# Optimization experiments

Measured on AMD Instinct MI355X. Metric: run time of the kernel, lower is better.

The kernel has to match this reference:

```python
import jax, jax.numpy as jnp
import numpy as np

DIM = 1024
HEADS = 16
DIM_HEAD = 64
INNER = HEADS * DIM_HEAD  # 1024
B, N = 2, 2048


def setup_inputs() -> dict:
    key = jax.random.key(0)
    ks = jax.random.split(key, 6)
    x = jax.random.normal(ks[0], (B, N, DIM), dtype=jnp.float32)
    rel_pos_bias = jax.random.normal(ks[1], (1, HEADS, N, N), dtype=jnp.float32)
    g = jnp.ones((DIM,), dtype=jnp.float32)
    # Linear weights stored torch-style as [out_features, in_features].
    # Note: original zero-inits Wo; we use small random values so outputs/grads are non-trivial.
    Wq = jax.random.normal(ks[2], (INNER, DIM), dtype=jnp.float32) * (DIM ** -0.5)
    Wkv = jax.random.normal(ks[3], (2 * INNER, DIM), dtype=jnp.float32) * (DIM ** -0.5)
    Wo = jax.random.normal(ks[4], (DIM, INNER), dtype=jnp.float32) * (INNER ** -0.5)
    return {"x": x, "rel_pos_bias": rel_pos_bias, "g": g, "Wq": Wq, "Wkv": Wkv, "Wo": Wo}


def reference(x, rel_pos_bias, g, Wq, Wkv, Wo):
    eps = 1e-5  # x is float32
    # Faithful to source: normalize over dim=1 (sequence axis), biased variance.
    mean = jnp.mean(x, axis=1, keepdims=True)          # [b, 1, d]
    var = jnp.var(x, axis=1, keepdims=True)            # [b, 1, d]
    xn = (x - mean) * jax.lax.rsqrt(jnp.maximum(var, eps)) * g

    q = xn @ Wq.T                                      # [b, n, inner]
    kv = xn @ Wkv.T                                    # [b, n, 2*inner]
    k, v = jnp.split(kv, 2, axis=-1)

    def to_heads(t):  # b n (h d) -> b h n d
        b, n, _ = t.shape
        return t.reshape(b, n, HEADS, DIM_HEAD).transpose(0, 2, 1, 3)

    q, k, v = to_heads(q), to_heads(k), to_heads(v)
    q = q * (DIM_HEAD ** -0.5)

    sim = jnp.einsum('bhid,bhjd->bhij', q, k) + rel_pos_bias  # [b, h, n, n]
    attn = jax.nn.softmax(sim, axis=-1)
    out = jnp.einsum('bhij,bhjd->bhid', attn, v)              # [b, h, n, d]
    out = out.transpose(0, 2, 1, 3).reshape(x.shape[0], x.shape[1], INNER)
    return out @ Wo.T                                         # [b, n, dim]
```

## Files before the change

kernel.cpp:

```cpp
#include <hip/hip_runtime.h>
#include <hip/hip_bf16.h>

typedef __bf16 bf16;
typedef __attribute__((ext_vector_type(8))) __bf16 bf16x8;
typedef __attribute__((ext_vector_type(4))) __bf16 bf16x4;
typedef __attribute__((ext_vector_type(4))) float f32x4;
typedef __attribute__((ext_vector_type(16))) float f32x16;
typedef __attribute__((ext_vector_type(4))) unsigned int u32x4;

#define DIMD  1024
#define SEQ   2048
#define BATCH 2
#define HEADS 16
#define INNER 1024
#define QKVN  3072
#define ROWS  (BATCH*SEQ)
#define LOG2E 1.44269504f

__global__ void ln_partial(const float* __restrict__ x,
                           float* __restrict__ psum, float* __restrict__ psq) {
    const int nc = blockIdx.x;
    const int b  = blockIdx.y;
    const int t  = threadIdx.x;
    const float* xp = x + ((size_t)b*SEQ + (size_t)nc*32)*DIMD;
    float s0=0,s1=0,s2=0,s3=0,q0=0,q1=0,q2=0,q3=0;
    for (int r=0; r<32; ++r) {
        const float* row = xp + (size_t)r*DIMD;
        float v0=row[t], v1=row[t+256], v2=row[t+512], v3=row[t+768];
        s0+=v0; q0+=v0*v0; s1+=v1; q1+=v1*v1;
        s2+=v2; q2+=v2*v2; s3+=v3; q3+=v3*v3;
    }
    float* ps = psum + ((size_t)b*64 + nc)*DIMD;
    float* pq = psq  + ((size_t)b*64 + nc)*DIMD;
    ps[t]=s0; ps[t+256]=s1; ps[t+512]=s2; ps[t+768]=s3;
    pq[t]=q0; pq[t+256]=q1; pq[t+512]=q2; pq[t+768]=q3;
}

__global__ void ln_finalize(const float* __restrict__ psum, const float* __restrict__ psq,
                            const float* __restrict__ g,
                            float* __restrict__ scale, float* __restrict__ shift) {
    const int d = blockIdx.x*256 + threadIdx.x;
    const int b = blockIdx.y;
    float s=0.f, q=0.f;
    for (int nc=0; nc<64; ++nc) {
        s += psum[((size_t)b*64+nc)*DIMD + d];
        q += psq [((size_t)b*64+nc)*DIMD + d];
    }
    const float inv_n = 1.f/(float)SEQ;
    float mean = s*inv_n;
    float var  = q*inv_n - mean*mean;
    var = fmaxf(var, 1e-5f);
    scale[b*DIMD+d] = g[d]*rsqrtf(var);
    shift[b*DIMD+d] = mean;
}

__global__ void ln_apply(const float* __restrict__ x,
                         const float* __restrict__ scale, const float* __restrict__ shift,
                         bf16* __restrict__ xn) {
    size_t idx = ((size_t)blockIdx.x*256 + threadIdx.x)*4;
    int b = (int)(idx >> 21);
    int d = (int)(idx & (DIMD-1));
    f32x4 v  = *reinterpret_cast<const f32x4*>(x + idx);
    f32x4 sc = *reinterpret_cast<const f32x4*>(scale + (size_t)b*DIMD + d);
    f32x4 sh = *reinterpret_cast<const f32x4*>(shift + (size_t)b*DIMD + d);
    bf16x4 o;
    o.x = (bf16)((v.x - sh.x)*sc.x);
    o.y = (bf16)((v.y - sh.y)*sc.y);
    o.z = (bf16)((v.z - sh.z)*sc.z);
    o.w = (bf16)((v.w - sh.w)*sc.w);
    *reinterpret_cast<bf16x4*>(xn + idx) = o;
}

__global__ void castk(const float* __restrict__ s, bf16* __restrict__ d, int n, float scl) {
    int i = (blockIdx.x*256 + threadIdx.x)*4;
    if (i >= n) return;
    f32x4 v = *reinterpret_cast<const f32x4*>(s + i);
    bf16x4 o; o.x=(bf16)(v.x*scl); o.y=(bf16)(v.y*scl); o.z=(bf16)(v.z*scl); o.w=(bf16)(v.w*scl);
    *reinterpret_cast<bf16x4*>(d + i) = o;
}

__device__ __forceinline__ void gload16(const void* g, void* l) {
    __builtin_amdgcn_global_load_lds(
        (const __attribute__((address_space(1))) unsigned int*)g,
        (__attribute__((address_space(3))) unsigned int*)l,
        16, 0, 0);
}

__device__ inline void store_out(float* p, float v) { *p = v; }
__device__ inline void store_out(bf16*  p, float v) { *p = (bf16)v; }

template <typename OT>
__global__ __launch_bounds__(256, 2)
void gemm_bt(const bf16* __restrict__ A, const bf16* __restrict__ B,
             OT* __restrict__ C, int M, int N, int K) {
    __shared__ bf16 As[128*64];
    __shared__ bf16 Bs[128*64];
    const int t = threadIdx.x;
    const int wave = t >> 6, lane = t & 63;
    const int wr = wave >> 1, wc = wave & 1;
    const int m0 = blockIdx.y*128, n0 = blockIdx.x*128;
    const int lr = lane & 15, lg = lane >> 4;
    const int srow = wave*32 + (lane>>3);
    const int scol = (lane&7)*8;

    f32x4 acc[4][4];
    #pragma unroll
    for (int i=0;i<4;++i)
        #pragma unroll
        for (int j=0;j<4;++j) acc[i][j] = (f32x4){0.f,0.f,0.f,0.f};

    for (int k0=0; k0<K; k0+=64) {
        #pragma unroll
        for (int i=0;i<4;++i) {
            gload16(A + (size_t)(m0+srow+8*i)*K + k0 + scol, As + (srow+8*i)*64 + scol);
            gload16(B + (size_t)(n0+srow+8*i)*K + k0 + scol, Bs + (srow+8*i)*64 + scol);
        }
        __syncthreads();
        #pragma unroll
        for (int kk=0; kk<2; ++kk) {
            bf16x8 a[4], b[4];
            #pragma unroll
            for (int mi=0;mi<4;++mi)
                a[mi] = *reinterpret_cast<const bf16x8*>(As + (wr*64+mi*16+lr)*64 + kk*32+lg*8);
            #pragma unroll
            for (int ni=0;ni<4;++ni)
                b[ni] = *reinterpret_cast<const bf16x8*>(Bs + (wc*64+ni*16+lr)*64 + kk*32+lg*8);
            #pragma unroll
            for (int mi=0;mi<4;++mi)
                #pragma unroll
                for (int ni=0;ni<4;++ni)
                    acc[mi][ni] = __builtin_amdgcn_mfma_f32_16x16x32_bf16(a[mi], b[ni], acc[mi][ni], 0, 0, 0);
        }
        __syncthreads();
    }
    #pragma unroll
    for (int mi=0;mi<4;++mi)
        #pragma unroll
        for (int ni=0;ni<4;++ni)
            #pragma unroll
            for (int r=0;r<4;++r) {
                int row = m0 + wr*64 + mi*16 + lg*4 + r;
                int col = n0 + wc*64 + ni*16 + lr;
                store_out(&C[(size_t)row*N + col], acc[mi][ni][r]);
            }
}

__global__ __launch_bounds__(256)
void transpose_v(const bf16* __restrict__ qkv, bf16* __restrict__ vT) {
    __shared__ bf16 tile[64][72];
    const int nt = blockIdx.x, h = blockIdx.y, b = blockIdx.z;
    const int t = threadIdx.x;
    const bf16* src = qkv + ((size_t)(b*SEQ + nt*64))*QKVN + 2*INNER + h*64;
    #pragma unroll
    for (int i=0;i<2;++i) {
        int c = t + 256*i, row = c>>3, col = (c&7)*8;
        *reinterpret_cast<bf16x8*>(&tile[row][col]) =
            *reinterpret_cast<const bf16x8*>(src + (size_t)row*QKVN + col);
    }
    __syncthreads();
    bf16* dst = vT + ((size_t)(b*HEADS + h))*64*SEQ + nt*64;
    #pragma unroll
    for (int i=0;i<2;++i) {
        int c = t + 256*i, d = c>>3, n0 = (c&7)*8;
        bf16x8 v;
        #pragma unroll
        for (int j=0;j<8;++j) v[j] = tile[n0+j][d];
        *reinterpret_cast<bf16x8*>(dst + (size_t)d*SEQ + n0) = v;
    }
}


__device__ __forceinline__ unsigned pk2(float a, float b) {
    union { bf16 h[2]; unsigned u; } x;
    x.h[0] = (bf16)a; x.h[1] = (bf16)b;
    return x.u;
}

#define ATTN_BARRIER()                                         \
    __builtin_amdgcn_sched_barrier(0);                         \
    asm volatile("s_waitcnt lgkmcnt(0)" ::: "memory");         \
    __builtin_amdgcn_s_barrier();                              \
    __builtin_amdgcn_sched_barrier(0)

#define ATTN_ITER(CUR, T)                                                          \
  {                                                                                \
              \
    if ((T)+1 < 32) {                                                              \
      *reinterpret_cast<bf16x8*>(&Ks[0][(CUR)^1][st_off])  = krA;                  \
      *reinterpret_cast<bf16x8*>(&Ks[1][(CUR)^1][st_off])  = krB;                  \
      *reinterpret_cast<bf16x8*>(&VTs[0][(CUR)^1][st_off]) = vrA;                  \
      *reinterpret_cast<bf16x8*>(&VTs[1][(CUR)^1][st_off]) = vrB;                  \
      _Pragma("unroll")                                                            \
      for (int i=0;i<4;++i)                                                        \
        *reinterpret_cast<f32x4*>(&BsL[(CUR)^1][bst[i]]) = breg[i];                \
    }                                                                              \
                      \
    if ((T)+2 < 32) {                                                              \
      krA = *reinterpret_cast<const bf16x8*>(kbase0 + (size_t)(((T)+2)*64+srow)*QKVN + scol);  \
      krB = *reinterpret_cast<const bf16x8*>(kbase1 + (size_t)(((T)+2)*64+srow)*QKVN + scol);  \
      vrA = *reinterpret_cast<const bf16x8*>(vtb0 + (size_t)srow*SEQ + ((T)+2)*64 + scol);     \
      vrB = *reinterpret_cast<const bf16x8*>(vtb1 + (size_t)srow*SEQ + ((T)+2)*64 + scol);     \
      _Pragma("unroll")                                                            \
      for (int i=0;i<4;++i)                                                        \
        breg[i] = *reinterpret_cast<const f32x4*>(bgl + (size_t)(32*i)*SEQ + ((T)+2)*64);      \
    }                                                                              \
                                    \
    f32x16 p0 = (f32x16)(0.0f), p1 = (f32x16)(0.0f);                               \
    __builtin_amdgcn_s_setprio(1);                                                 \
    _Pragma("unroll")                                                              \
    for (int s=0;s<4;++s) {                                                        \
      bf16x8 kf0 = *reinterpret_cast<const bf16x8*>(&myK[(CUR)*4096 + koff[0][s]]); \
      p0 = __builtin_amdgcn_mfma_f32_32x32x16_bf16(kf0, qf[s], p0, 0,0,0);         \
      bf16x8 kf1 = *reinterpret_cast<const bf16x8*>(&myK[(CUR)*4096 + koff[1][s]]); \
      p1 = __builtin_amdgcn_mfma_f32_32x32x16_bf16(kf1, qf[s], p1, 0,0,0);         \
    }                                                                              \
    __builtin_amdgcn_s_setprio(0);                                                 \
                              \
    f32x4 bb0[4], bb1[4];                                                          \
    _Pragma("unroll")                                                              \
    for (int rr=0;rr<4;++rr) {                                                     \
      bb0[rr] = *reinterpret_cast<const f32x4*>(&BsL[CUR][brd[0][rr]]);            \
      bb1[rr] = *reinterpret_cast<const f32x4*>(&BsL[CUR][brd[1][rr]]);            \
    }                                                                              \
            \
    float v0[16], v1[16];                                                          \
    _Pragma("unroll")                                                              \
    for (int r=0;r<16;++r) {                                                       \
      v0[r] = __builtin_fmaf(bb0[r>>2][r&3], LOG2E, p0[r]);                        \
      v1[r] = __builtin_fmaf(bb1[r>>2][r&3], LOG2E, p1[r]);                        \
    }                                                                              \
    float mx[8];                                                                   \
    _Pragma("unroll")                                                              \
    for (int i=0;i<8;++i)                                                          \
      mx[i] = fmaxf(fmaxf(v0[i], v0[i+8]), fmaxf(v1[i], v1[i+8]));                 \
    _Pragma("unroll")                                                              \
    for (int i=0;i<4;++i) mx[i] = fmaxf(mx[i], mx[i+4]);                           \
    float vmax = fmaxf(fmaxf(mx[0],mx[2]), fmaxf(mx[1],mx[3]));                    \
    vmax = fmaxf(vmax, __shfl_xor(vmax, 32));                                      \
    if (!__all(vmax <= m + 11.5f)) {                                               \
      float mnew = fmaxf(m, vmax);                                                 \
      float sc = __builtin_amdgcn_exp2f(m - mnew);                                 \
      m = mnew; l *= sc;                                                           \
      _Pragma("unroll")                                                            \
      for (int r=0;r<16;++r) {                                                     \
        float scr = __shfl(sc, (r&3)+8*(r>>2)+4*hi);                               \
        accO0[r] *= scr; accO1[r] *= scr;                                          \
      }                                                                            \
    }                                                                              \
    float e0[16], e1[16];                                                          \
    _Pragma("unroll")                                                              \
    for (int r=0;r<16;++r) {                                                       \
      e0[r] = __builtin_amdgcn_exp2f(v0[r] - m);                                   \
      e1[r] = __builtin_amdgcn_exp2f(v1[r] - m);                                   \
    }                                                                              \
    float sm[8];                                                                   \
    _Pragma("unroll")                                                              \
    for (int i=0;i<8;++i) sm[i] = (e0[i]+e0[i+8]) + (e1[i]+e1[i+8]);               \
    _Pragma("unroll")                                                              \
    for (int i=0;i<4;++i) sm[i] += sm[i+4];                                        \
    float rsum = (sm[0]+sm[2]) + (sm[1]+sm[3]);                                    \
    rsum += __shfl_xor(rsum, 32);                                                  \
    l += rsum;                                                                     \
           \
    unsigned W0[4][2], W1[4][2];                                                   \
    _Pragma("unroll")                                                              \
    for (int rr=0;rr<4;++rr) {                                                     \
      W0[rr][0] = pk2(e0[4*rr+0], e0[4*rr+1]);                                     \
      W0[rr][1] = pk2(e0[4*rr+2], e0[4*rr+3]);                                     \
      W1[rr][0] = pk2(e1[4*rr+0], e1[4*rr+1]);                                     \
      W1[rr][1] = pk2(e1[4*rr+2], e1[4*rr+3]);                                     \
    }                                                                              \
                               \
    bf16x8 pa[4];                                                                  \
    _Pragma("unroll")                                                              \
    for (int s4=0;s4<4;++s4) {                                                     \
      unsigned u[4];                                                               \
      _Pragma("unroll")                                                            \
      for (int hh=0;hh<2;++hh) {                                                   \
        unsigned a0 = (s4>>1) ? W1[2*(s4&1)  ][hh] : W0[2*(s4&1)  ][hh];           \
        unsigned a1 = (s4>>1) ? W1[2*(s4&1)+1][hh] : W0[2*(s4&1)+1][hh];           \
        unsigned X = hi ? a0 : a1;                                                 \
        unsigned R = (unsigned)__shfl_xor((int)X, 32);                             \
        u[hh]   = hi ? R  : a0;                                                    \
        u[2+hh] = hi ? a1 : R;                                                     \
      }                                                                            \
      u32x4 uv = {u[0], u[1], u[2], u[3]};                                         \
      pa[s4] = __builtin_bit_cast(bf16x8, uv);                                     \
    }                                                                              \
                                                                        \
    __builtin_amdgcn_s_setprio(1);                                                 \
    _Pragma("unroll")                                                              \
    for (int s4=0;s4<4;++s4) {                                                     \
      bf16x8 vfa = *reinterpret_cast<const bf16x8*>(&myV[(CUR)*4096 + voff[0][s4]]); \
      accO0 = __builtin_amdgcn_mfma_f32_32x32x16_bf16(pa[s4], vfa, accO0, 0,0,0);  \
      bf16x8 vfb = *reinterpret_cast<const bf16x8*>(&myV[(CUR)*4096 + voff[1][s4]]); \
      accO1 = __builtin_amdgcn_mfma_f32_32x32x16_bf16(pa[s4], vfb, accO1, 0,0,0);  \
    }                                                                              \
    __builtin_amdgcn_s_setprio(0);                                                 \
    ATTN_BARRIER();                                                                \
  }

__global__ __launch_bounds__(512, 1)
void attn_kernel(const bf16* __restrict__ qkv, const bf16* __restrict__ vTg,
                 const float* __restrict__ bias, bf16* __restrict__ oh) {
    __shared__ bf16 Ks[2][2][64*64];
    __shared__ bf16 VTs[2][2][64*64];
    __shared__ float BsL[2][128*64];

    const int qt = blockIdx.x, h = blockIdx.y;
    const int t = threadIdx.x;
    const int w = t >> 6, lane = t & 63;
    const int wb = w >> 2;
    const int wq = w & 3;
    const int ql = lane & 31, hi = lane >> 5;
    const int q0 = qt*128;

    int koff[2][4], voff[2][4];
    #pragma unroll
    for (int B2=0;B2<2;++B2)
        #pragma unroll
        for (int s=0;s<4;++s) {
            koff[B2][s] = (32*B2+ql)*64 + (((2*s+hi) ^ (ql&7))*8);
            voff[B2][s] = (32*B2+ql)*64 + (((2*s+hi) ^ (ql&7))*8);
        }
    bf16* myK = (bf16*)Ks[wb];
    bf16* myV = (bf16*)VTs[wb];

    int bst[4];
    {
        int rlow = t>>4;
        int swg  = ((t&15) ^ (rlow&15))*4;
        #pragma unroll
        for (int i=0;i<4;++i)
            bst[i] = (32*i + rlow)*64 + swg;
    }
    int brd[2][4];
    #pragma unroll
    for (int B2=0;B2<2;++B2)
        #pragma unroll
        for (int rr=0;rr<4;++rr)
            brd[B2][rr] = (wq*32+ql)*64 + (((8*B2+2*rr+hi) ^ (ql&15))*4);

    const int srow = t>>3;
    const int scol = (t&7)*8;
    const int st_off = srow*64 + (((t&7) ^ (srow&7))*8);

    const bf16* qrow = qkv + ((size_t)(wb*SEQ + q0 + wq*32 + ql))*QKVN + h*64 + hi*8;
    bf16x8 qf[4];
    #pragma unroll
    for (int s=0;s<4;++s)
        qf[s] = *reinterpret_cast<const bf16x8*>(qrow + 16*s);

    const bf16* kbase0 = qkv + INNER + h*64;
    const bf16* kbase1 = qkv + (size_t)SEQ*QKVN + INNER + h*64;
    const bf16* vtb0   = vTg + (size_t)h*64*SEQ;
    const bf16* vtb1   = vTg + (size_t)(HEADS + h)*64*SEQ;
    const float* bgl = bias + ((size_t)h*SEQ + (size_t)(q0 + (t>>4)))*SEQ + 4*(t&15);

    bf16x8 krA, krB, vrA, vrB;
    f32x4 breg[4];

    *reinterpret_cast<bf16x8*>(&Ks[0][0][st_off]) =
        *reinterpret_cast<const bf16x8*>(kbase0 + (size_t)srow*QKVN + scol);
    *reinterpret_cast<bf16x8*>(&Ks[1][0][st_off]) =
        *reinterpret_cast<const bf16x8*>(kbase1 + (size_t)srow*QKVN + scol);
    *reinterpret_cast<bf16x8*>(&VTs[0][0][st_off]) =
        *reinterpret_cast<const bf16x8*>(vtb0 + (size_t)srow*SEQ + scol);
    *reinterpret_cast<bf16x8*>(&VTs[1][0][st_off]) =
        *reinterpret_cast<const bf16x8*>(vtb1 + (size_t)srow*SEQ + scol);
    #pragma unroll
    for (int i=0;i<4;++i)
        breg[i] = *reinterpret_cast<const f32x4*>(bgl + (size_t)(32*i)*SEQ);
    #pragma unroll
    for (int i=0;i<4;++i)
        *reinterpret_cast<f32x4*>(&BsL[0][bst[i]]) = breg[i];
    krA = *reinterpret_cast<const bf16x8*>(kbase0 + (size_t)(64+srow)*QKVN + scol);
    krB = *reinterpret_cast<const bf16x8*>(kbase1 + (size_t)(64+srow)*QKVN + scol);
    vrA = *reinterpret_cast<const bf16x8*>(vtb0 + (size_t)srow*SEQ + 64 + scol);
    vrB = *reinterpret_cast<const bf16x8*>(vtb1 + (size_t)srow*SEQ + 64 + scol);
    #pragma unroll
    for (int i=0;i<4;++i)
        breg[i] = *reinterpret_cast<const f32x4*>(bgl + (size_t)(32*i)*SEQ + 64);
    ATTN_BARRIER();

    float m = -__builtin_inff();
    float l = 0.f;
    f32x16 accO0 = (f32x16)(0.0f), accO1 = (f32x16)(0.0f);

    for (int t2 = 0; t2 < 32; t2 += 2) {
        ATTN_ITER(0, t2);
        ATTN_ITER(1, t2+1);
    }

    float linv = 1.f/l;
    bf16* ob = oh + ((size_t)(wb*SEQ + q0 + wq*32))*INNER + h*64 + ql;
    #pragma unroll
    for (int r=0;r<16;++r) {
        int qoff = (r&3) + 8*(r>>2) + 4*hi;
        float li = __shfl(linv, qoff);
        ob[(size_t)qoff*INNER]      = (bf16)(accO0[r]*li);
        ob[(size_t)qoff*INNER + 32] = (bf16)(accO1[r]*li);
    }
}

extern "C" void kernel_launch(void* const* d_in, const int* in_sizes, int n_in,
                              void* d_out, int out_size, void* d_ws, size_t ws_size,
                              hipStream_t stream) {
    const float* x    = (const float*)d_in[0];
    const float* bias = (const float*)d_in[1];
    const float* g    = (const float*)d_in[2];
    const float* Wq   = (const float*)d_in[3];
    const float* Wkv  = (const float*)d_in[4];
    const float* Wo   = (const float*)d_in[5];
    float* out = (float*)d_out;

    char* ws = (char*)d_ws;
    bf16*  xn    = (bf16*)(ws);
    bf16*  vT    = (bf16*)(ws);
    bf16*  wqkv  = (bf16*)(ws + 8388608);
    bf16*  wo    = (bf16*)(ws + 14680064);
    bf16*  qkv   = (bf16*)(ws + 16777216);
    bf16*  oh    = (bf16*)(ws + 41943040);
    float* psum  = (float*)(ws + 50331648);
    float* psq   = (float*)(ws + 50855936);
    float* scale = (float*)(ws + 51380224);
    float* shift = (float*)(ws + 51388416);

    ln_partial <<<dim3(64,2), 256, 0, stream>>>(x, psum, psq);
    ln_finalize<<<dim3(4,2),  256, 0, stream>>>(psum, psq, g, scale, shift);
    ln_apply   <<<dim3(4096), 256, 0, stream>>>(x, scale, shift, xn);

    castk<<<dim3(1024), 256, 0, stream>>>(Wq,  wqkv,           1048576, 0.125f*LOG2E);
    castk<<<dim3(2048), 256, 0, stream>>>(Wkv, wqkv + 1048576, 2097152, 1.0f);
    castk<<<dim3(1024), 256, 0, stream>>>(Wo,  wo,             1048576, 1.0f);

    gemm_bt<bf16><<<dim3(24,32), 256, 0, stream>>>(xn, wqkv, qkv, ROWS, QKVN, DIMD);

    transpose_v<<<dim3(32,16,2), 256, 0, stream>>>(qkv, vT);

    attn_kernel<<<dim3(16,16), 512, 0, stream>>>(qkv, vT, bias, oh);

    gemm_bt<float><<<dim3(8,32), 256, 0, stream>>>(oh, wo, out, ROWS, INNER, INNER);
}
```

Baseline: 181.6 us.

## Stage attention K/V/bias tiles with direct global-to-LDS loads and fuse weight casts

The attention kernel no longer copies K, V^T and bias tiles through registers into LDS. It issues global_load_lds DMA into the swizzled double buffers one tile ahead, and each iteration's barrier now waits on vmcnt as well. This frees registers and removes LDS store instructions, but the prefetch distance shrinks from two tiles to one, so every iteration must drain its global loads. Separately, the three weight-cast launches are merged into one kernel to save launch overhead.

```diff
diff --git a/kernel.cpp b/kernel.cpp
--- a/kernel.cpp
+++ b/kernel.cpp
@@ -71,12 +71,19 @@
     *reinterpret_cast<bf16x4*>(xn + idx) = o;
 }
 
-__global__ void castk(const float* __restrict__ s, bf16* __restrict__ d, int n, float scl) {
+__global__ void castk_all(const float* __restrict__ Wq, const float* __restrict__ Wkv,
+                          const float* __restrict__ Wo,
+                          bf16* __restrict__ wqkv, bf16* __restrict__ wo, float qs) {
     int i = (blockIdx.x*256 + threadIdx.x)*4;
-    if (i >= n) return;
-    f32x4 v = *reinterpret_cast<const f32x4*>(s + i);
-    bf16x4 o; o.x=(bf16)(v.x*scl); o.y=(bf16)(v.y*scl); o.z=(bf16)(v.z*scl); o.w=(bf16)(v.w*scl);
-    *reinterpret_cast<bf16x4*>(d + i) = o;
+    f32x4 v; bf16* dst;
+    if (i < 1048576)      { v = *reinterpret_cast<const f32x4*>(Wq + i);
+                            v.x*=qs; v.y*=qs; v.z*=qs; v.w*=qs; dst = wqkv + i; }
+    else if (i < 3145728) { v = *reinterpret_cast<const f32x4*>(Wkv + (i-1048576));
+                            dst = wqkv + i; }
+    else                  { v = *reinterpret_cast<const f32x4*>(Wo + (i-3145728));
+                            dst = wo + (i-3145728); }
+    bf16x4 o; o.x=(bf16)v.x; o.y=(bf16)v.y; o.z=(bf16)v.z; o.w=(bf16)v.w;
+    *reinterpret_cast<bf16x4*>(dst) = o;
 }
 
 __device__ __forceinline__ void gload16(const void* g, void* l) {
@@ -176,34 +183,27 @@
     return x.u;
 }
 
-#define ATTN_BARRIER()                                         \
-    __builtin_amdgcn_sched_barrier(0);                         \
-    asm volatile("s_waitcnt lgkmcnt(0)" ::: "memory");         \
-    __builtin_amdgcn_s_barrier();                              \
+#define ATTN_BARRIER_VM()                                                \
+    __builtin_amdgcn_sched_barrier(0);                                   \
+    asm volatile("s_waitcnt vmcnt(0) lgkmcnt(0)" ::: "memory");          \
+    __builtin_amdgcn_s_barrier();                                        \
     __builtin_amdgcn_sched_barrier(0)
+
+#define STAGE(BUF, TT)                                                           \
+  {                                                                              \
+    gload16(kA + (size_t)(TT)*64*QKVN, &Ks[0][BUF][t*8]);                        \
+    gload16(kB + (size_t)(TT)*64*QKVN, &Ks[1][BUF][t*8]);                        \
+    gload16(vA + (TT)*64,              &VTs[0][BUF][t*8]);                       \
+    gload16(vB + (TT)*64,              &VTs[1][BUF][t*8]);                       \
+    _Pragma("unroll")                                                            \
+    for (int i_=0;i_<4;++i_)                                                     \
+        gload16(bptr + (size_t)(32*i_)*SEQ + (TT)*64, &BsL[BUF][t*4 + i_*2048]); \
+  }
 
 #define ATTN_ITER(CUR, T)                                                          \
   {                                                                                \
-              \
-    if ((T)+1 < 32) {                                                              \
-      *reinterpret_cast<bf16x8*>(&Ks[0][(CUR)^1][st_off])  = krA;                  \
-      *reinterpret_cast<bf16x8*>(&Ks[1][(CUR)^1][st_off])  = krB;                  \
-      *reinterpret_cast<bf16x8*>(&VTs[0][(CUR)^1][st_off]) = vrA;                  \
-      *reinterpret_cast<bf16x8*>(&VTs[1][(CUR)^1][st_off]) = vrB;                  \
-      _Pragma("unroll")                                                            \
-      for (int i=0;i<4;++i)                                                        \
-        *reinterpret_cast<f32x4*>(&BsL[(CUR)^1][bst[i]]) = breg[i];                \
-    }                                                                              \
-                      \
-    if ((T)+2 < 32) {                                                              \
-      krA = *reinterpret_cast<const bf16x8*>(kbase0 + (size_t)(((T)+2)*64+srow)*QKVN + scol);  \
-      krB = *reinterpret_cast<const bf16x8*>(kbase1 + (size_t)(((T)+2)*64+srow)*QKVN + scol);  \
-      vrA = *reinterpret_cast<const bf16x8*>(vtb0 + (size_t)srow*SEQ + ((T)+2)*64 + scol);     \
-      vrB = *reinterpret_cast<const bf16x8*>(vtb1 + (size_t)srow*SEQ + ((T)+2)*64 + scol);     \
-      _Pragma("unroll")                                                            \
-      for (int i=0;i<4;++i)                                                        \
-        breg[i] = *reinterpret_cast<const f32x4*>(bgl + (size_t)(32*i)*SEQ + ((T)+2)*64);      \
-    }                                                                              \
+     \
+    if ((T)+1 < 32) STAGE((CUR)^1, (T)+1);                                         \
                                     \
     f32x16 p0 = (f32x16)(0.0f), p1 = (f32x16)(0.0f);                               \
     __builtin_amdgcn_s_setprio(1);                                                 \
@@ -297,7 +297,7 @@
       accO1 = __builtin_amdgcn_mfma_f32_32x32x16_bf16(pa[s4], vfb, accO1, 0,0,0);  \
     }                                                                              \
     __builtin_amdgcn_s_setprio(0);                                                 \
-    ATTN_BARRIER();                                                                \
+    ATTN_BARRIER_VM();                                                             \
   }
 
 __global__ __launch_bounds__(512, 1)
@@ -326,14 +326,6 @@
     bf16* myK = (bf16*)Ks[wb];
     bf16* myV = (bf16*)VTs[wb];
 
-    int bst[4];
-    {
-        int rlow = t>>4;
-        int swg  = ((t&15) ^ (rlow&15))*4;
-        #pragma unroll
-        for (int i=0;i<4;++i)
-            bst[i] = (32*i + rlow)*64 + swg;
-    }
     int brd[2][4];
     #pragma unroll
     for (int B2=0;B2<2;++B2)
@@ -341,47 +333,26 @@
         for (int rr=0;rr<4;++rr)
             brd[B2][rr] = (wq*32+ql)*64 + (((8*B2+2*rr+hi) ^ (ql&15))*4);
 
-    const int srow = t>>3;
-    const int scol = (t&7)*8;
-    const int st_off = srow*64 + (((t&7) ^ (srow&7))*8);
-
-    const bf16* qrow = qkv + ((size_t)(wb*SEQ + q0 + wq*32 + ql))*QKVN + h*64 + hi*8;
-    bf16x8 qf[4];
-    #pragma unroll
-    for (int s=0;s<4;++s)
-        qf[s] = *reinterpret_cast<const bf16x8*>(qrow + 16*s);
-
+    const int swz8k = (((t&7) ^ ((t>>3)&7))*8);
     const bf16* kbase0 = qkv + INNER + h*64;
     const bf16* kbase1 = qkv + (size_t)SEQ*QKVN + INNER + h*64;
     const bf16* vtb0   = vTg + (size_t)h*64*SEQ;
     const bf16* vtb1   = vTg + (size_t)(HEADS + h)*64*SEQ;
-    const float* bgl = bias + ((size_t)h*SEQ + (size_t)(q0 + (t>>4)))*SEQ + 4*(t&15);
-
-    bf16x8 krA, krB, vrA, vrB;
-    f32x4 breg[4];
-
-    *reinterpret_cast<bf16x8*>(&Ks[0][0][st_off]) =
-        *reinterpret_cast<const bf16x8*>(kbase0 + (size_t)srow*QKVN + scol);
-    *reinterpret_cast<bf16x8*>(&Ks[1][0][st_off]) =
-        *reinterpret_cast<const bf16x8*>(kbase1 + (size_t)srow*QKVN + scol);
-    *reinterpret_cast<bf16x8*>(&VTs[0][0][st_off]) =
-        *reinterpret_cast<const bf16x8*>(vtb0 + (size_t)srow*SEQ + scol);
-    *reinterpret_cast<bf16x8*>(&VTs[1][0][st_off]) =
-        *reinterpret_cast<const bf16x8*>(vtb1 + (size_t)srow*SEQ + scol);
-    #pragma unroll
-    for (int i=0;i<4;++i)
-        breg[i] = *reinterpret_cast<const f32x4*>(bgl + (size_t)(32*i)*SEQ);
-    #pragma unroll
-    for (int i=0;i<4;++i)
-        *reinterpret_cast<f32x4*>(&BsL[0][bst[i]]) = breg[i];
-    krA = *reinterpret_cast<const bf16x8*>(kbase0 + (size_t)(64+srow)*QKVN + scol);
-    krB = *reinterpret_cast<const bf16x8*>(kbase1 + (size_t)(64+srow)*QKVN + scol);
-    vrA = *reinterpret_cast<const bf16x8*>(vtb0 + (size_t)srow*SEQ + 64 + scol);
-    vrB = *reinterpret_cast<const bf16x8*>(vtb1 + (size_t)srow*SEQ + 64 + scol);
-    #pragma unroll
-    for (int i=0;i<4;++i)
-        breg[i] = *reinterpret_cast<const f32x4*>(bgl + (size_t)(32*i)*SEQ + 64);
-    ATTN_BARRIER();
+    const bf16* kA = kbase0 + (size_t)(t>>3)*QKVN + swz8k;
+    const bf16* kB = kbase1 + (size_t)(t>>3)*QKVN + swz8k;
+    const bf16* vA = vtb0 + (size_t)(t>>3)*SEQ + swz8k;
+    const bf16* vB = vtb1 + (size_t)(t>>3)*SEQ + swz8k;
+    const float* bptr = bias + ((size_t)h*SEQ + (size_t)(q0 + (t>>4)))*SEQ
+                              + (((t&15) ^ ((t>>4)&15))*4);
+
+    const bf16* qrow = qkv + ((size_t)(wb*SEQ + q0 + wq*32 + ql))*QKVN + h*64 + hi*8;
+    bf16x8 qf[4];
+    #pragma unroll
+    for (int s=0;s<4;++s)
+        qf[s] = *reinterpret_cast<const bf16x8*>(qrow + 16*s);
+
+    STAGE(0, 0);
+    ATTN_BARRIER_VM();
 
     float m = -__builtin_inff();
     float l = 0.f;
@@ -430,9 +401,7 @@
     ln_finalize<<<dim3(4,2),  256, 0, stream>>>(psum, psq, g, scale, shift);
     ln_apply   <<<dim3(4096), 256, 0, stream>>>(x, scale, shift, xn);
 
-    castk<<<dim3(1024), 256, 0, stream>>>(Wq,  wqkv,           1048576, 0.125f*LOG2E);
-    castk<<<dim3(2048), 256, 0, stream>>>(Wkv, wqkv + 1048576, 2097152, 1.0f);
-    castk<<<dim3(1024), 256, 0, stream>>>(Wo,  wo,             1048576, 1.0f);
+    castk_all<<<dim3(4096), 256, 0, stream>>>(Wq, Wkv, Wo, wqkv, wo, 0.125f*LOG2E);
 
     gemm_bt<bf16><<<dim3(24,32), 256, 0, stream>>>(xn, wqkv, qkv, ROWS, QKVN, DIMD);
 
```

Result: slower. 193.6 us (+6.6%).
